# Kernel optimization log

Hardware: AMD Instinct MI355X
Metric: run time of the kernel (lower is better)

The kernel has to match this reference:

```python
import jax, jax.numpy as jnp
import numpy as np

N = 100000   # total nodes
E = 1600000  # total edges
B = 256      # graphs per batch
F_NODE, F_EDGE, H = 35, 10, 64
N_CONV = 3
IN_DIM = 2 * H + F_EDGE  # 138
EPS = 1e-5


def setup_inputs() -> dict:
    key = jax.random.key(0)
    ks = jax.random.split(key, 16)
    node_features = jax.random.normal(ks[0], (N, F_NODE), dtype=jnp.float32)
    edge_index = jax.random.randint(ks[1], (2, E), 0, N, dtype=jnp.int64)
    edge_features = jax.random.uniform(ks[2], (E, F_EDGE), dtype=jnp.float32)
    graph_index = jnp.sort(jax.random.randint(ks[3], (N,), 0, B, dtype=jnp.int64))
    s = lambda fan_in: 1.0 / np.sqrt(fan_in)
    embed_w = jax.random.uniform(ks[4], (F_NODE, H), jnp.float32, -s(F_NODE), s(F_NODE))
    embed_b = jax.random.uniform(ks[5], (H,), jnp.float32, -s(F_NODE), s(F_NODE))
    gate_w = jax.random.uniform(ks[6], (N_CONV, IN_DIM, H), jnp.float32, -s(IN_DIM), s(IN_DIM))
    gate_b = jax.random.uniform(ks[7], (N_CONV, H), jnp.float32, -s(IN_DIM), s(IN_DIM))
    cand_w = jax.random.uniform(ks[8], (N_CONV, IN_DIM, H), jnp.float32, -s(IN_DIM), s(IN_DIM))
    cand_b = jax.random.uniform(ks[9], (N_CONV, H), jnp.float32, -s(IN_DIM), s(IN_DIM))
    bn_g = jnp.ones((N_CONV, H), dtype=jnp.float32)
    bn_b = jnp.zeros((N_CONV, H), dtype=jnp.float32)
    mlp_w1 = jax.random.uniform(ks[10], (H, 128), jnp.float32, -s(H), s(H))
    mlp_b1 = jax.random.uniform(ks[11], (128,), jnp.float32, -s(H), s(H))
    mlp_w2 = jax.random.uniform(ks[12], (128, 64), jnp.float32, -s(128), s(128))
    mlp_b2 = jax.random.uniform(ks[13], (64,), jnp.float32, -s(128), s(128))
    mlp_w3 = jax.random.uniform(ks[14], (64, 1), jnp.float32, -s(64), s(64))
    mlp_b3 = jax.random.uniform(ks[15], (1,), jnp.float32, -s(64), s(64))
    return dict(node_features=node_features, edge_index=edge_index,
                edge_features=edge_features, graph_index=graph_index,
                embed_w=embed_w, embed_b=embed_b,
                gate_w=gate_w, gate_b=gate_b, cand_w=cand_w, cand_b=cand_b,
                bn_g=bn_g, bn_b=bn_b,
                mlp_w1=mlp_w1, mlp_b1=mlp_b1, mlp_w2=mlp_w2, mlp_b2=mlp_b2,
                mlp_w3=mlp_w3, mlp_b3=mlp_b3)


def _conv(h, src, dst, edge_feat, gw, gb, cw, cb, gamma, beta):
    # gather -> concat -> gated message
    z = jnp.concatenate([h[src], h[dst], edge_feat], axis=1)  # [E, 2H+F_edge]
    g = jax.nn.sigmoid(z @ gw + gb)
    c = jax.nn.softplus(z @ cw + cb)
    m = g * c
    # scatter-add onto source nodes
    agg = jax.ops.segment_sum(m, src, num_segments=h.shape[0])
    # BatchNorm1d (training-mode batch stats, biased variance)
    mu = agg.mean(axis=0)
    var = agg.var(axis=0)
    agg_bn = (agg - mu) * jax.lax.rsqrt(var + EPS) * gamma + beta
    return jax.nn.softplus(h + agg_bn)


def reference(node_features, edge_index, edge_features, graph_index,
              embed_w, embed_b, gate_w, gate_b, cand_w, cand_b, bn_g, bn_b,
              mlp_w1, mlp_b1, mlp_w2, mlp_b2, mlp_w3, mlp_b3):
    src, dst = edge_index[0], edge_index[1]
    h = node_features @ embed_w + embed_b  # [N, H]
    for i in range(N_CONV):
        h = _conv(h, src, dst, edge_features,
                  gate_w[i], gate_b[i], cand_w[i], cand_b[i], bn_g[i], bn_b[i])
    # mean pool per graph (B is static = 256)
    pooled = jax.ops.segment_sum(h, graph_index, num_segments=B)
    counts = jax.ops.segment_sum(jnp.ones((h.shape[0],), h.dtype), graph_index, num_segments=B)
    pooled = pooled / jnp.clip(counts, 1.0, None)[:, None]
    x = jax.nn.softplus(pooled @ mlp_w1 + mlp_b1)
    x = jax.nn.softplus(x @ mlp_w2 + mlp_b2)
    return (x @ mlp_w3 + mlp_b3)[:, 0]  # [B]
```

## Files before the change

kernel.cpp:

```cpp
#include <hip/hip_runtime.h>
#include <hip/hip_bf16.h>

#define NN 100000
#define EE 1600000
#define BB 256
#define F_NODE 35
#define F_EDGE 10
#define HH 64
#define IN_DIM 138
#define N_CONV 3
#define EPSBN 1e-5f
#define NB1 ((NN + 255) / 256)

#define NBLK 4000
#define NGROUPS 25
#define SUBLEN 100
#define EPB 400
#define EFSTR 12

typedef _Float16 half8 __attribute__((ext_vector_type(8)));
typedef float floatx4 __attribute__((ext_vector_type(4)));

__device__ __forceinline__ float softplus_fast(float x) {
    return fmaxf(x, 0.0f) + __logf(1.0f + __expf(-fabsf(x)));
}
__device__ __forceinline__ float sigmoid_fast(float x) {
    return __builtin_amdgcn_rcpf(1.0f + __expf(-x));
}

__global__ __launch_bounds__(256)
void hist_rank_kernel(const int* __restrict__ src, int* __restrict__ cnt,
                      int* __restrict__ rank) {
    int e = blockIdx.x * 256 + threadIdx.x;
    rank[e] = atomicAdd(&cnt[src[e]], 1);
}

__global__ __launch_bounds__(256)
void scan1_kernel(int* __restrict__ cnt, int* __restrict__ bsum, int n) {
    __shared__ int ls[256];
    int t = threadIdx.x;
    int i = blockIdx.x * 256 + t;
    int v = (i < n) ? cnt[i] : 0;
    ls[t] = v;
    __syncthreads();
#pragma unroll
    for (int off = 1; off < 256; off <<= 1) {
        int add = (t >= off) ? ls[t - off] : 0;
        __syncthreads();
        ls[t] += add;
        __syncthreads();
    }
    if (i < n) cnt[i] = ls[t] - v;
    if (t == 255) bsum[blockIdx.x] = ls[255];
}

__global__ __launch_bounds__(512)
void scan2_kernel(int* __restrict__ bsum, int nb) {
    __shared__ int ls[512];
    int t = threadIdx.x;
    int v = (t < nb) ? bsum[t] : 0;
    ls[t] = v;
    __syncthreads();
#pragma unroll
    for (int off = 1; off < 512; off <<= 1) {
        int add = (t >= off) ? ls[t - off] : 0;
        __syncthreads();
        ls[t] += add;
        __syncthreads();
    }
    if (t < nb) bsum[t] = ls[t] - v;
}

__global__ __launch_bounds__(256)
void perm_kernel(const int* __restrict__ src, const int* __restrict__ rank,
                 const int* __restrict__ offs, const int* __restrict__ bsum,
                 int* __restrict__ perm) {
    int e = blockIdx.x * 256 + threadIdx.x;
    int s = src[e];
    perm[offs[s] + bsum[s >> 8] + rank[e]] = e;
}

__global__ __launch_bounds__(256)
void gather_kernel(const int* __restrict__ perm,
                   const int* __restrict__ src, const int* __restrict__ dst,
                   const float* __restrict__ ef,
                   int* __restrict__ ssorted, int* __restrict__ dsorted,
                   _Float16* __restrict__ ef16) {
    int pos = blockIdx.x * 256 + threadIdx.x;
    int e = perm[pos];
    ssorted[pos] = src[e];
    dsorted[pos] = dst[e];
    const float2* efe = (const float2*)(ef + (size_t)e * F_EDGE);
    uint* op = (uint*)(ef16 + (size_t)pos * EFSTR);
#pragma unroll
    for (int i = 0; i < 5; i++) {
        float2 v = efe[i];
        _Float16 h0 = (_Float16)v.x;
        _Float16 h1 = (_Float16)v.y;
        op[i] = (uint)*(unsigned short*)&h0 | ((uint)*(unsigned short*)&h1 << 16);
    }
    op[5] = 0u;
}

__global__ __launch_bounds__(256)
void prep_w_kernel(const float* __restrict__ gw, const float* __restrict__ cw,
                   _Float16* __restrict__ wT) {
    int idx = blockIdx.x * 256 + threadIdx.x;
    if (idx >= 3 * 128 * 160) return;
    int k = idx % 160;
    int n = (idx / 160) & 127;
    int layer = idx / (160 * 128);
    float v = 0.f;
    if (k < IN_DIM)
        v = (n < 64) ? gw[layer * IN_DIM * HH + k * HH + n]
                     : cw[layer * IN_DIM * HH + k * HH + (n - 64)];
    wT[idx] = (_Float16)v;
}

__global__ __launch_bounds__(256)
void embed_kernel(const float* __restrict__ nf, const float* __restrict__ w,
                  const float* __restrict__ bias, float* __restrict__ h,
                  _Float16* __restrict__ h16, int n) {
    __shared__ float wl[F_NODE * HH];
    int tid = threadIdx.x;
    for (int i = tid; i < F_NODE * HH; i += 256) wl[i] = w[i];
    __syncthreads();
    int idx = blockIdx.x * 256 + tid;
    int node = idx >> 6, j = idx & 63;
    if (node >= n) return;
    float acc = bias[j];
    const float* row = nf + node * F_NODE;
#pragma unroll
    for (int k = 0; k < F_NODE; k++) acc += row[k] * wl[k * HH + j];
    h[idx] = acc;
    h16[idx] = (_Float16)acc;
}

__device__ __forceinline__ void load_A(const _Float16* __restrict__ h16,
                                       const _Float16* __restrict__ ef16,
                                       int s, int d, int eg, int quad,
                                       uint4& A0, uint4& A1, uint4& A2, uint4& A3,
                                       uint4& A4) {
    const uint4* hs = (const uint4*)(h16 + (size_t)s * HH);
    const uint4* hd = (const uint4*)(h16 + (size_t)d * HH);
    A0 = hs[quad];
    A1 = hs[quad + 4];
    A2 = hd[quad];
    A3 = hd[quad + 4];
    uint4 z; z.x = z.y = z.z = z.w = 0u;
    A4 = z;
    const _Float16* p = ef16 + (size_t)eg * EFSTR;
    if (quad == 0) {
        uint2 a = *(const uint2*)p;
        uint2 b = *(const uint2*)(p + 4);
        A4.x = a.x; A4.y = a.y; A4.z = b.x; A4.w = b.y;
    } else if (quad == 1) {
        uint2 a = *(const uint2*)(p + 8);
        A4.x = a.x; A4.y = a.y;
    }
}

__global__ __launch_bounds__(128, 3)
void edge_conv_mfma(const _Float16* __restrict__ h16,
                    const int* __restrict__ esrc,
                    const int* __restrict__ edst,
                    const _Float16* __restrict__ ef16,
                    const _Float16* __restrict__ wT,
                    const float* __restrict__ gb, const float* __restrict__ cb,
                    float* __restrict__ agg) {
    int lane = threadIdx.x & 63;
    int w = threadIdx.x >> 6;
    int quad = lane >> 4, n15 = lane & 15;
    int base = blockIdx.x * EPB + ((n15 >> 2) * SUBLEN) + (n15 & 3);

    int tg = 2 * w;
    half8 B[4][5];
#pragma unroll
    for (int j = 0; j < 2; j++) {
        const _Float16* wrg = wT + ((tg + j) * 16 + n15) * 160 + quad * 8;
        const _Float16* wrc = wT + ((4 + tg + j) * 16 + n15) * 160 + quad * 8;
#pragma unroll
        for (int ks = 0; ks < 5; ks++) {
            B[j][ks]     = *(const half8*)(wrg + ks * 32);
            B[2 + j][ks] = *(const half8*)(wrc + ks * 32);
        }
    }
    float gb0 = gb[tg * 16 + n15], gb1 = gb[(tg + 1) * 16 + n15];
    float cb0 = cb[tg * 16 + n15], cb1 = cb[(tg + 1) * 16 + n15];
    int colbase = tg * 16 + n15;

    int sprev = -1;
    float am0 = 0.f, am1 = 0.f;

    int eg = base;
    int s = esrc[eg], d = edst[eg];
    uint4 A0, A1, A2, A3, A4;
    load_A(h16, ef16, s, d, eg, quad, A0, A1, A2, A3, A4);
    int egn = base + 4;
    int sn = esrc[egn], dn = edst[egn];

    for (int g = 0; g < NGROUPS; g++) {
        int s_cur = s;

        floatx4 acc[4];
#pragma unroll
        for (int t = 0; t < 4; t++) acc[t] = (floatx4){0.f, 0.f, 0.f, 0.f};

        half8 a0 = __builtin_bit_cast(half8, A0);
        half8 a1 = __builtin_bit_cast(half8, A1);
        half8 a2 = __builtin_bit_cast(half8, A2);
        half8 a3 = __builtin_bit_cast(half8, A3);
        half8 a4 = __builtin_bit_cast(half8, A4);
#pragma unroll
        for (int t = 0; t < 4; t++) acc[t] = __builtin_amdgcn_mfma_f32_16x16x32_f16(a0, B[t][0], acc[t], 0, 0, 0);
#pragma unroll
        for (int t = 0; t < 4; t++) acc[t] = __builtin_amdgcn_mfma_f32_16x16x32_f16(a1, B[t][1], acc[t], 0, 0, 0);
#pragma unroll
        for (int t = 0; t < 4; t++) acc[t] = __builtin_amdgcn_mfma_f32_16x16x32_f16(a2, B[t][2], acc[t], 0, 0, 0);
#pragma unroll
        for (int t = 0; t < 4; t++) acc[t] = __builtin_amdgcn_mfma_f32_16x16x32_f16(a3, B[t][3], acc[t], 0, 0, 0);
#pragma unroll
        for (int t = 0; t < 4; t++) acc[t] = __builtin_amdgcn_mfma_f32_16x16x32_f16(a4, B[t][4], acc[t], 0, 0, 0);

        int egc = base + ((g + 1 < NGROUPS) ? (g + 1) * 4 : g * 4);
        load_A(h16, ef16, sn, dn, egc, quad, A0, A1, A2, A3, A4);
        s = sn; d = dn;
        int eg2 = base + ((g + 2 < NGROUPS) ? (g + 2) * 4 : (NGROUPS - 1) * 4);
        sn = esrc[eg2]; dn = edst[eg2];

#pragma unroll
        for (int r = 0; r < 4; r++) {
            int sr = __shfl(s_cur, quad * 4 + r, 64);
            if (sr != sprev) {
                if (sprev >= 0) {
                    float* p = agg + (size_t)sprev * HH + colbase;
                    atomicAdd(p, am0);
                    atomicAdd(p + 16, am1);
                }
                sprev = sr;
                am0 = am1 = 0.f;
            }
            am0 += sigmoid_fast(acc[0][r] + gb0) * softplus_fast(acc[2][r] + cb0);
            am1 += sigmoid_fast(acc[1][r] + gb1) * softplus_fast(acc[3][r] + cb1);
        }
    }
    if (sprev >= 0) {
        float* p = agg + (size_t)sprev * HH + colbase;
        atomicAdd(p, am0);
        atomicAdd(p + 16, am1);
    }
}

__global__ __launch_bounds__(256)
void bn_stats_kernel(const float* __restrict__ agg, float* __restrict__ stats, int total) {
    __shared__ float ls[256], lss[256];
    int tid = threadIdx.x;
    float s = 0.f, ss = 0.f;
    for (int idx = blockIdx.x * 256 + tid; idx < total; idx += gridDim.x * 256) {
        float v = agg[idx];
        s += v;
        ss += v * v;
    }
    ls[tid] = s;
    lss[tid] = ss;
    __syncthreads();
    if (tid < 64) {
        s = ls[tid] + ls[tid + 64] + ls[tid + 128] + ls[tid + 192];
        ss = lss[tid] + lss[tid + 64] + lss[tid + 128] + lss[tid + 192];
        atomicAdd(&stats[tid], s);
        atomicAdd(&stats[64 + tid], ss);
    }
}

__global__ __launch_bounds__(256)
void bn_update_kernel(float* __restrict__ h, _Float16* __restrict__ h16,
                      float* __restrict__ agg,
                      const float* __restrict__ stats,
                      const float* __restrict__ g, const float* __restrict__ b,
                      int total, float invN) {
    int idx = blockIdx.x * 256 + threadIdx.x;
    if (idx >= total) return;
    int j = idx & 63;
    float mu = stats[j] * invN;
    float var = stats[64 + j] * invN - mu * mu;
    var = fmaxf(var, 0.0f);
    float scale = g[j] * rsqrtf(var + EPSBN);
    float a = agg[idx];
    agg[idx] = 0.f;
    float v = h[idx] + (a - mu) * scale + b[j];
    float hv = softplus_fast(v);
    h[idx] = hv;
    h16[idx] = (_Float16)hv;
}

__global__ __launch_bounds__(256)
void pool_kernel(const float* __restrict__ h, const int* __restrict__ gi,
                 float* __restrict__ pool, float* __restrict__ counts, int n) {
    int tid = threadIdx.x;
    int grp = tid >> 6;
    int j = tid & 63;
    int n0 = blockIdx.x * 64 + grp * 16;
    if (n0 >= n) return;
    int nend = n0 + 16; if (nend > n) nend = n;
    int gprev = gi[n0];
    float a = 0.f;
    int cnt = 0;
    for (int nn = n0; nn < nend; nn++) {
        int gg = gi[nn];
        if (gg != gprev) {
            atomicAdd(&pool[gprev * 64 + j], a);
            if (j == 0) atomicAdd(&counts[gprev], (float)cnt);
            a = 0.f; cnt = 0; gprev = gg;
        }
        a += h[(size_t)nn * 64 + j];
        cnt++;
    }
    atomicAdd(&pool[gprev * 64 + j], a);
    if (j == 0) atomicAdd(&counts[gprev], (float)cnt);
}

__global__ __launch_bounds__(128)
void mlp_kernel(const float* __restrict__ pool, const float* __restrict__ counts,
                const float* __restrict__ w1, const float* __restrict__ b1,
                const float* __restrict__ w2, const float* __restrict__ b2,
                const float* __restrict__ w3, const float* __restrict__ b3,
                float* __restrict__ out) {
    __shared__ float x0[64], x1[128], x2[64];
    int b = blockIdx.x, t = threadIdx.x;
    if (t < 64) {
        float c = counts[b];
        c = c < 1.f ? 1.f : c;
        x0[t] = pool[b * 64 + t] / c;
    }
    __syncthreads();
    {
        float acc = 0.f;
#pragma unroll
        for (int k = 0; k < 64; k++) acc += x0[k] * w1[k * 128 + t];
        x1[t] = softplus_fast(acc + b1[t]);
    }
    __syncthreads();
    if (t < 64) {
        float acc = 0.f;
#pragma unroll
        for (int k = 0; k < 128; k++) acc += x1[k] * w2[k * 64 + t];
        x2[t] = softplus_fast(acc + b2[t]);
    }
    __syncthreads();
    if (t == 0) {
        float acc = 0.f;
        for (int k = 0; k < 64; k++) acc += x2[k] * w3[k];
        out[b] = acc + b3[0];
    }
}

extern "C" void kernel_launch(void* const* d_in, const int* in_sizes, int n_in,
                              void* d_out, int out_size, void* d_ws, size_t ws_size,
                              hipStream_t stream) {
    const float* nf      = (const float*)d_in[0];
    const int*   ei      = (const int*)d_in[1];
    const float* ef      = (const float*)d_in[2];
    const int*   gi      = (const int*)d_in[3];
    const float* embed_w = (const float*)d_in[4];
    const float* embed_b = (const float*)d_in[5];
    const float* gate_w  = (const float*)d_in[6];
    const float* gate_b  = (const float*)d_in[7];
    const float* cand_w  = (const float*)d_in[8];
    const float* cand_b  = (const float*)d_in[9];
    const float* bn_g    = (const float*)d_in[10];
    const float* bn_b    = (const float*)d_in[11];
    const float* w1      = (const float*)d_in[12];
    const float* b1      = (const float*)d_in[13];
    const float* w2      = (const float*)d_in[14];
    const float* b2      = (const float*)d_in[15];
    const float* w3      = (const float*)d_in[16];
    const float* b3      = (const float*)d_in[17];
    float* out = (float*)d_out;

    const int NH = NN * HH;
    char* p = (char*)d_ws;
    int*       offs    = (int*)p;              p += (size_t)NN * 4;
    float*     agg     = (float*)p;            p += (size_t)NH * 4;
    float*     stats   = (float*)p;            p += 3 * 128 * 4;
    float*     pool    = (float*)p;            p += (size_t)BB * HH * 4;
    float*     counts  = (float*)p;            p += (size_t)BB * 4;
    size_t zero_bytes = (size_t)(p - (char*)d_ws);
    float*     h       = (float*)p;            p += (size_t)NH * 4;
    _Float16*  h16     = (_Float16*)p;         p += (size_t)NH * 2;
    int*       ssorted = (int*)p;              p += (size_t)EE * 4;
    int*       dsorted = (int*)p;              p += (size_t)EE * 4;
    _Float16*  ef16    = (_Float16*)p;         p += (size_t)EE * EFSTR * 2;
    int*       perm    = (int*)p;              p += (size_t)EE * 4;
    int*       rank    = (int*)p;              p += (size_t)EE * 4;
    _Float16*  wTall   = (_Float16*)p;         p += (size_t)3 * 128 * 160 * 2;
    int*       bsum    = (int*)p;              p += 512 * 4;

    const int* src = ei;
    const int* dst = ei + EE;

    hipMemsetAsync(d_ws, 0, zero_bytes, stream);

    hist_rank_kernel<<<EE / 256, 256, 0, stream>>>(src, offs, rank);
    prep_w_kernel<<<(3 * 128 * 160 + 255) / 256, 256, 0, stream>>>(gate_w, cand_w, wTall);
    scan1_kernel<<<NB1, 256, 0, stream>>>(offs, bsum, NN);
    scan2_kernel<<<1, 512, 0, stream>>>(bsum, NB1);
    perm_kernel<<<EE / 256, 256, 0, stream>>>(src, rank, offs, bsum, perm);
    gather_kernel<<<EE / 256, 256, 0, stream>>>(perm, src, dst, ef, ssorted, dsorted, ef16);

    embed_kernel<<<NH / 256, 256, 0, stream>>>(nf, embed_w, embed_b, h, h16, NN);

    for (int i = 0; i < N_CONV; i++) {
        edge_conv_mfma<<<NBLK, 128, 0, stream>>>(
            h16, ssorted, dsorted, ef16,
            wTall + (size_t)i * 128 * 160,
            gate_b + i * HH, cand_b + i * HH, agg);
        bn_stats_kernel<<<512, 256, 0, stream>>>(agg, stats + i * 128, NH);
        bn_update_kernel<<<NH / 256, 256, 0, stream>>>(
            h, h16, agg, stats + i * 128, bn_g + i * HH, bn_b + i * HH, NH, 1.0f / (float)NN);
    }

    pool_kernel<<<(NN + 63) / 64, 256, 0, stream>>>(h, gi, pool, counts, NN);
    mlp_kernel<<<BB, 128, 0, stream>>>(pool, counts, w1, b1, w2, b2, w3, b3, out);
}
```

Measured before the change: 883.0 us.

## Drop fp32 node state, prefetch two edge groups ahead, cheaper activations

Removes the fp32 copy of the node state, so the residual, BN update and pooling read and write only the fp16 buffer. The edge conv kernel now keeps two groups of gathered rows in flight, seeds the accumulators with the biases, and computes sigmoid and softplus with raw exp2/log builtins. Edge blocking changes to 5000 blocks of 320 edges. This cuts memory traffic and ALU work, but the residual path now carries fp16 rounding error across layers, and the unguarded softplus can overflow for large inputs.

```diff
diff --git a/kernel.cpp b/kernel.cpp
--- a/kernel.cpp
+++ b/kernel.cpp
@@ -12,20 +12,28 @@
 #define EPSBN 1e-5f
 #define NB1 ((NN + 255) / 256)
 
-#define NBLK 4000
-#define NGROUPS 25
-#define SUBLEN 100
-#define EPB 400
+#define NBLK 5000
+#define NGROUPS 20
+#define SUBLEN 80
+#define EPB 320
 #define EFSTR 12
+
+#define LOG2E 1.442695041f
+#define LN2   0.6931471806f
 
 typedef _Float16 half8 __attribute__((ext_vector_type(8)));
 typedef float floatx4 __attribute__((ext_vector_type(4)));
 
 __device__ __forceinline__ float softplus_fast(float x) {
-    return fmaxf(x, 0.0f) + __logf(1.0f + __expf(-fabsf(x)));
-}
-__device__ __forceinline__ float sigmoid_fast(float x) {
-    return __builtin_amdgcn_rcpf(1.0f + __expf(-x));
+    float t = __builtin_amdgcn_exp2f(LOG2E * x);
+    return LN2 * __builtin_amdgcn_logf(1.0f + t);
+}
+__device__ __forceinline__ float mpair(float g, float c) {
+    float tg = __builtin_amdgcn_exp2f(-LOG2E * g);
+    float sig = __builtin_amdgcn_rcpf(1.0f + tg);
+    float tc = __builtin_amdgcn_exp2f(LOG2E * c);
+    float sp = LN2 * __builtin_amdgcn_logf(1.0f + tc);
+    return sig * sp;
 }
 
 __global__ __launch_bounds__(256)
@@ -119,8 +127,7 @@
 
 __global__ __launch_bounds__(256)
 void embed_kernel(const float* __restrict__ nf, const float* __restrict__ w,
-                  const float* __restrict__ bias, float* __restrict__ h,
-                  _Float16* __restrict__ h16, int n) {
+                  const float* __restrict__ bias, _Float16* __restrict__ h16, int n) {
     __shared__ float wl[F_NODE * HH];
     int tid = threadIdx.x;
     for (int i = tid; i < F_NODE * HH; i += 256) wl[i] = w[i];
@@ -132,31 +139,29 @@
     const float* row = nf + node * F_NODE;
 #pragma unroll
     for (int k = 0; k < F_NODE; k++) acc += row[k] * wl[k * HH + j];
-    h[idx] = acc;
     h16[idx] = (_Float16)acc;
 }
 
-__device__ __forceinline__ void load_A(const _Float16* __restrict__ h16,
-                                       const _Float16* __restrict__ ef16,
-                                       int s, int d, int eg, int quad,
-                                       uint4& A0, uint4& A1, uint4& A2, uint4& A3,
-                                       uint4& A4) {
+__device__ __forceinline__ void loadA(uint4* A,
+                                      const _Float16* __restrict__ h16,
+                                      const _Float16* __restrict__ ef16,
+                                      int s, int d, int eg, int quad) {
     const uint4* hs = (const uint4*)(h16 + (size_t)s * HH);
     const uint4* hd = (const uint4*)(h16 + (size_t)d * HH);
-    A0 = hs[quad];
-    A1 = hs[quad + 4];
-    A2 = hd[quad];
-    A3 = hd[quad + 4];
+    A[0] = hs[quad];
+    A[1] = hs[quad + 4];
+    A[2] = hd[quad];
+    A[3] = hd[quad + 4];
     uint4 z; z.x = z.y = z.z = z.w = 0u;
-    A4 = z;
+    A[4] = z;
     const _Float16* p = ef16 + (size_t)eg * EFSTR;
     if (quad == 0) {
         uint2 a = *(const uint2*)p;
         uint2 b = *(const uint2*)(p + 4);
-        A4.x = a.x; A4.y = a.y; A4.z = b.x; A4.w = b.y;
+        A[4].x = a.x; A[4].y = a.y; A[4].z = b.x; A[4].w = b.y;
     } else if (quad == 1) {
         uint2 a = *(const uint2*)(p + 8);
-        A4.x = a.x; A4.y = a.y;
+        A[4].x = a.x; A[4].y = a.y;
     }
 }
 
@@ -192,56 +197,62 @@
     int sprev = -1;
     float am0 = 0.f, am1 = 0.f;
 
-    int eg = base;
-    int s = esrc[eg], d = edst[eg];
-    uint4 A0, A1, A2, A3, A4;
-    load_A(h16, ef16, s, d, eg, quad, A0, A1, A2, A3, A4);
-    int egn = base + 4;
-    int sn = esrc[egn], dn = edst[egn];
-
-    for (int g = 0; g < NGROUPS; g++) {
-        int s_cur = s;
-
-        floatx4 acc[4];
-#pragma unroll
-        for (int t = 0; t < 4; t++) acc[t] = (floatx4){0.f, 0.f, 0.f, 0.f};
-
-        half8 a0 = __builtin_bit_cast(half8, A0);
-        half8 a1 = __builtin_bit_cast(half8, A1);
-        half8 a2 = __builtin_bit_cast(half8, A2);
-        half8 a3 = __builtin_bit_cast(half8, A3);
-        half8 a4 = __builtin_bit_cast(half8, A4);
-#pragma unroll
-        for (int t = 0; t < 4; t++) acc[t] = __builtin_amdgcn_mfma_f32_16x16x32_f16(a0, B[t][0], acc[t], 0, 0, 0);
-#pragma unroll
-        for (int t = 0; t < 4; t++) acc[t] = __builtin_amdgcn_mfma_f32_16x16x32_f16(a1, B[t][1], acc[t], 0, 0, 0);
-#pragma unroll
-        for (int t = 0; t < 4; t++) acc[t] = __builtin_amdgcn_mfma_f32_16x16x32_f16(a2, B[t][2], acc[t], 0, 0, 0);
-#pragma unroll
-        for (int t = 0; t < 4; t++) acc[t] = __builtin_amdgcn_mfma_f32_16x16x32_f16(a3, B[t][3], acc[t], 0, 0, 0);
-#pragma unroll
-        for (int t = 0; t < 4; t++) acc[t] = __builtin_amdgcn_mfma_f32_16x16x32_f16(a4, B[t][4], acc[t], 0, 0, 0);
-
-        int egc = base + ((g + 1 < NGROUPS) ? (g + 1) * 4 : g * 4);
-        load_A(h16, ef16, sn, dn, egc, quad, A0, A1, A2, A3, A4);
-        s = sn; d = dn;
-        int eg2 = base + ((g + 2 < NGROUPS) ? (g + 2) * 4 : (NGROUPS - 1) * 4);
-        sn = esrc[eg2]; dn = edst[eg2];
-
-#pragma unroll
-        for (int r = 0; r < 4; r++) {
-            int sr = __shfl(s_cur, quad * 4 + r, 64);
-            if (sr != sprev) {
-                if (sprev >= 0) {
-                    float* p = agg + (size_t)sprev * HH + colbase;
-                    atomicAdd(p, am0);
-                    atomicAdd(p + 16, am1);
+    uint4 A[2][5];
+    int sg2[2], sp[2], dp[2];
+    {
+        int e0 = base, e1 = base + 4;
+        int s0 = esrc[e0], d0 = edst[e0];
+        int s1 = esrc[e1], d1 = edst[e1];
+        loadA(A[0], h16, ef16, s0, d0, e0, quad);
+        loadA(A[1], h16, ef16, s1, d1, e1, quad);
+        sg2[0] = s0; sg2[1] = s1;
+        int e2 = base + 8, e3 = base + 12;
+        sp[0] = esrc[e2]; dp[0] = edst[e2];
+        sp[1] = esrc[e3]; dp[1] = edst[e3];
+    }
+
+    for (int g = 0; g < NGROUPS; g += 2) {
+#pragma unroll
+        for (int k = 0; k < 2; k++) {
+            int gk = g + k;
+            int s_cur = sg2[k];
+
+            floatx4 acc[4];
+            acc[0] = (floatx4){gb0, gb0, gb0, gb0};
+            acc[1] = (floatx4){gb1, gb1, gb1, gb1};
+            acc[2] = (floatx4){cb0, cb0, cb0, cb0};
+            acc[3] = (floatx4){cb1, cb1, cb1, cb1};
+
+#pragma unroll
+            for (int ks = 0; ks < 5; ks++) {
+                half8 a = __builtin_bit_cast(half8, A[k][ks]);
+#pragma unroll
+                for (int t = 0; t < 4; t++)
+                    acc[t] = __builtin_amdgcn_mfma_f32_16x16x32_f16(a, B[t][ks], acc[t], 0, 0, 0);
+            }
+
+            int gl = (gk + 2 < NGROUPS) ? gk + 2 : NGROUPS - 1;
+            loadA(A[k], h16, ef16, sp[k], dp[k], base + gl * 4, quad);
+            sg2[k] = sp[k];
+            int gp = (gk + 4 < NGROUPS) ? gk + 4 : NGROUPS - 1;
+            int ep = base + gp * 4;
+            sp[k] = esrc[ep]; dp[k] = edst[ep];
+
+#pragma unroll
+            for (int r = 0; r < 4; r++) {
+                int sr = __shfl(s_cur, quad * 4 + r, 64);
+                if (sr != sprev) {
+                    if (sprev >= 0) {
+                        float* p = agg + (size_t)sprev * HH + colbase;
+                        atomicAdd(p, am0);
+                        atomicAdd(p + 16, am1);
+                    }
+                    sprev = sr;
+                    am0 = am1 = 0.f;
                 }
-                sprev = sr;
-                am0 = am1 = 0.f;
+                am0 += mpair(acc[0][r], acc[2][r]);
+                am1 += mpair(acc[1][r], acc[3][r]);
             }
-            am0 += sigmoid_fast(acc[0][r] + gb0) * softplus_fast(acc[2][r] + cb0);
-            am1 += sigmoid_fast(acc[1][r] + gb1) * softplus_fast(acc[3][r] + cb1);
         }
     }
     if (sprev >= 0) {
@@ -273,7 +284,7 @@
 }
 
 __global__ __launch_bounds__(256)
-void bn_update_kernel(float* __restrict__ h, _Float16* __restrict__ h16,
+void bn_update_kernel(_Float16* __restrict__ h16,
                       float* __restrict__ agg,
                       const float* __restrict__ stats,
                       const float* __restrict__ g, const float* __restrict__ b,
@@ -287,14 +298,12 @@
     float scale = g[j] * rsqrtf(var + EPSBN);
     float a = agg[idx];
     agg[idx] = 0.f;
-    float v = h[idx] + (a - mu) * scale + b[j];
-    float hv = softplus_fast(v);
-    h[idx] = hv;
-    h16[idx] = (_Float16)hv;
-}
-
-__global__ __launch_bounds__(256)
-void pool_kernel(const float* __restrict__ h, const int* __restrict__ gi,
+    float v = (float)h16[idx] + (a - mu) * scale + b[j];
+    h16[idx] = (_Float16)softplus_fast(v);
+}
+
+__global__ __launch_bounds__(256)
+void pool_kernel(const _Float16* __restrict__ h16, const int* __restrict__ gi,
                  float* __restrict__ pool, float* __restrict__ counts, int n) {
     int tid = threadIdx.x;
     int grp = tid >> 6;
@@ -312,7 +321,7 @@
             if (j == 0) atomicAdd(&counts[gprev], (float)cnt);
             a = 0.f; cnt = 0; gprev = gg;
         }
-        a += h[(size_t)nn * 64 + j];
+        a += (float)h16[(size_t)nn * 64 + j];
         cnt++;
     }
     atomicAdd(&pool[gprev * 64 + j], a);
@@ -385,7 +394,6 @@
     float*     pool    = (float*)p;            p += (size_t)BB * HH * 4;
     float*     counts  = (float*)p;            p += (size_t)BB * 4;
     size_t zero_bytes = (size_t)(p - (char*)d_ws);
-    float*     h       = (float*)p;            p += (size_t)NH * 4;
     _Float16*  h16     = (_Float16*)p;         p += (size_t)NH * 2;
     int*       ssorted = (int*)p;              p += (size_t)EE * 4;
     int*       dsorted = (int*)p;              p += (size_t)EE * 4;
@@ -407,7 +415,7 @@
     perm_kernel<<<EE / 256, 256, 0, stream>>>(src, rank, offs, bsum, perm);
     gather_kernel<<<EE / 256, 256, 0, stream>>>(perm, src, dst, ef, ssorted, dsorted, ef16);
 
-    embed_kernel<<<NH / 256, 256, 0, stream>>>(nf, embed_w, embed_b, h, h16, NN);
+    embed_kernel<<<NH / 256, 256, 0, stream>>>(nf, embed_w, embed_b, h16, NN);
 
     for (int i = 0; i < N_CONV; i++) {
         edge_conv_mfma<<<NBLK, 128, 0, stream>>>(
@@ -416,9 +424,9 @@
             gate_b + i * HH, cand_b + i * HH, agg);
         bn_stats_kernel<<<512, 256, 0, stream>>>(agg, stats + i * 128, NH);
         bn_update_kernel<<<NH / 256, 256, 0, stream>>>(
-            h, h16, agg, stats + i * 128, bn_g + i * HH, bn_b + i * HH, NH, 1.0f / (float)NN);
-    }
-
-    pool_kernel<<<(NN + 63) / 64, 256, 0, stream>>>(h, gi, pool, counts, NN);
+            h16, agg, stats + i * 128, bn_g + i * HH, bn_b + i * HH, NH, 1.0f / (float)NN);
+    }
+
+    pool_kernel<<<(NN + 63) / 64, 256, 0, stream>>>(h16, gi, pool, counts, NN);
     mlp_kernel<<<BB, 128, 0, stream>>>(pool, counts, w1, b1, w2, b2, w3, b3, out);
 }
```

Result: slower. 1.225 ms (+38.7%).
